# Kernel optimization log

Measured on AMD Instinct MI355X. Metric: run time of the kernel, lower is better.

## Reference

```python
import jax, jax.numpy as jnp
import numpy as np

MAX_SEGMENTS = 196
MAX_PIX = 400        # max_pixels_per_segment
C = 3                # n_channels
EMBED = 768


def setup_inputs() -> dict:
    key = jax.random.key(0)
    k1, k2, k3, k4 = jax.random.split(key, 4)
    B, H, W = 64, 224, 224
    img = jax.random.normal(k1, (B, C, H, W), jnp.float32)
    segments = jax.random.randint(k2, (B, H, W), 0, MAX_SEGMENTS).astype(jnp.int32)
    fan_in = C * MAX_PIX
    Wp = jax.random.normal(k3, (EMBED, fan_in), jnp.float32) / np.sqrt(fan_in)
    b = jax.random.normal(k4, (EMBED,), jnp.float32) * 0.01
    return {"img": img, "segments": segments, "W": Wp, "b": b}


def _gather_pad(img_flat, seg_flat):
    # img_flat: [C, P], seg_flat: [P] int32. Builds [S, C*MAX_PIX] padded buffer.
    P = seg_flat.shape[0]
    order = jnp.argsort(seg_flat, stable=True)          # stable -> keeps scan order (matches torch truncation)
    s = seg_flat[order]                                  # sorted segment ids, [P]
    counts = jnp.zeros((MAX_SEGMENTS,), jnp.int32).at[seg_flat].add(1)
    starts = jnp.concatenate([jnp.zeros((1,), jnp.int32),
                              jnp.cumsum(counts)[:-1].astype(jnp.int32)])
    rank = jnp.arange(P, dtype=jnp.int32) - starts[s]    # within-segment position
    valid = rank < MAX_PIX                               # truncate overly large segments
    rank_c = jnp.where(valid, rank, 0)
    vals = jnp.where(valid[:, None], img_flat.T[order], 0.0)  # [P, C]
    buf = jnp.zeros((MAX_SEGMENTS, C, MAX_PIX), img_flat.dtype)
    buf = buf.at[s, :, rank_c].add(vals)                 # invalid rows add zeros -> no-op
    # torch does pixels_in_segment.flatten() on (C, MAX_PIX) -> channel-major layout
    return buf.reshape(MAX_SEGMENTS, C * MAX_PIX)


def reference(img, segments, W, b):
    B = img.shape[0]
    img_flat = img.reshape(B, C, -1)          # [B, C, H*W]
    seg_flat = segments.reshape(B, -1)        # [B, H*W]
    feats = jax.vmap(_gather_pad)(img_flat, seg_flat)   # [B, S, C*MAX_PIX]
    return jnp.einsum('bsf,ef->bse', feats, W) + b      # nn.Linear
```

## Files before the change

kernel.cpp:

```cpp
#include <hip/hip_runtime.h>
#include <hip/hip_bf16.h>

#define B_      64
#define C_      3
#define H_      224
#define W_      224
#define P_      (H_*W_)
#define S_      196
#define MAXPIX  400
#define E_      768
#define K_      1200
#define KP_     1216
#define CHUNK_  512
#define NCH_    (P_/CHUNK_)
#define M_      (B_*S_)

typedef __attribute__((ext_vector_type(8))) short short8;
typedef __attribute__((ext_vector_type(4))) float f32x4;

__device__ inline unsigned short f2bf(float f) {
  union { float f; unsigned int u; } x; x.f = f;
  return (unsigned short)((x.u + 0x7fffu + ((x.u >> 16) & 1u)) >> 16);
}

__device__ inline int xcd_chunk(int wg, int nwg) {
  int q = nwg >> 3;
  return (wg & 7) * q + (wg >> 3);
}

__global__ void wconv_k(const float* __restrict__ Wf, unsigned short* __restrict__ Wb) {
  int idx = blockIdx.x * 256 + threadIdx.x;
  int e = idx / KP_, k = idx - e * KP_;
  float v = (k < K_) ? Wf[e * K_ + k] : 0.f;
  Wb[idx] = f2bf(v);
}

__global__ __launch_bounds__(512) void rank_k(const int* __restrict__ seg,
                                              int* __restrict__ hist,
                                              unsigned short* __restrict__ rloc) {
  int b = blockIdx.x / NCH_, ch = blockIdx.x % NCH_;
  int tid = threadIdx.x, wave = tid >> 6, lane = tid & 63;
  int p = ch * CHUNK_ + tid;
  int s = seg[b * P_ + p];

  __shared__ int lhist[8][S_];
  for (int i = tid; i < 8 * S_; i += 512) ((int*)lhist)[i] = 0;
  __syncthreads();

  int r = 0;
  #pragma unroll 1
  for (int j = 0; j < 64; ++j) {
    int sj = __shfl(s, j);
    r += (j < lane && sj == s) ? 1 : 0;
  }
  atomicAdd(&lhist[wave][s], 1);
  __syncthreads();

  int off = 0;
  for (int w2 = 0; w2 < wave; ++w2) off += lhist[w2][s];
  rloc[b * P_ + p] = (unsigned short)(off + r);

  if (tid < S_) {
    int t = 0;
    #pragma unroll
    for (int w2 = 0; w2 < 8; ++w2) t += lhist[w2][tid];
    hist[(b * NCH_ + ch) * S_ + tid] = t;
  }
}

__global__ __launch_bounds__(128) void prefix_k(int* __restrict__ hist, int* __restrict__ cnts) {
  int b = blockIdx.x / S_, s = blockIdx.x % S_;
  int t = threadIdx.x;
  __shared__ int sc[128];
  int v = (t < NCH_) ? hist[(b * NCH_ + t) * S_ + s] : 0;
  sc[t] = v;
  __syncthreads();
  #pragma unroll
  for (int off = 1; off < 128; off <<= 1) {
    int x = (t >= off) ? sc[t - off] : 0;
    __syncthreads();
    sc[t] += x;
    __syncthreads();
  }
  if (t < NCH_) hist[(b * NCH_ + t) * S_ + s] = sc[t] - v;
  if (t == NCH_ - 1) {
    int tot = sc[t];
    cnts[b * S_ + s] = tot < MAXPIX ? tot : MAXPIX;
  }
}

__global__ __launch_bounds__(256) void scatter_inv_k(const int* __restrict__ seg,
                                                     const int* __restrict__ starts,
                                                     const unsigned short* __restrict__ rloc,
                                                     unsigned short* __restrict__ inv) {
  int wg = xcd_chunk(blockIdx.x, B_ * (P_ / 256));
  int b = wg / (P_ / 256);
  int p = (wg % (P_ / 256)) * 256 + threadIdx.x;
  int s = seg[b * P_ + p];
  int rank = starts[(b * NCH_ + (p >> 9)) * S_ + s] + rloc[b * P_ + p];
  if (rank < MAXPIX)
    inv[(b * S_ + s) * MAXPIX + rank] = (unsigned short)p;
}

__global__ __launch_bounds__(256) void gather_k(const float* __restrict__ img,
                                                const unsigned short* __restrict__ inv,
                                                const int* __restrict__ cnts,
                                                unsigned short* __restrict__ feats) {
  int wg = xcd_chunk(blockIdx.x, M_);
  int b = wg / S_, s = wg % S_;
  int t = threadIdx.x;
  int cnt = cnts[b * S_ + s];
  const unsigned short* invrow = inv + (size_t)(b * S_ + s) * MAXPIX;
  unsigned short* frow = feats + (size_t)(b * S_ + s) * KP_;
  #pragma unroll
  for (int c = 0; c < C_; ++c) {
    const float* ic = img + ((size_t)b * C_ + c) * P_;
    for (int r = t; r < MAXPIX; r += 256) {
      int p = invrow[r];
      float v = (r < cnt) ? ic[p] : 0.f;
      frow[c * MAXPIX + r] = f2bf(v);
    }
  }
  if (t < KP_ - K_) frow[K_ + t] = 0;
}

__global__ __launch_bounds__(256) void gemm_k(const unsigned short* __restrict__ A,
                                              const unsigned short* __restrict__ Bw,
                                              const float* __restrict__ bias,
                                              float* __restrict__ out) {
  int bid;
  {
    int wg = blockIdx.x, q = 588 / 8, r = 588 % 8;
    int xcd = wg % 8, idx = wg / 8;
    bid = (xcd < r) ? xcd * (q + 1) + idx : r * (q + 1) + (xcd - r) * q + idx;
  }
  const int nb = bid % (E_ / 128);
  const int mb = bid / (E_ / 128);
  const int tid = threadIdx.x;
  const int w = tid >> 6, l = tid & 63;
  const int wr = w >> 1, wc = w & 1;

  __shared__ __align__(16) unsigned short As[128 * 32];
  __shared__ __align__(16) unsigned short Bs[128 * 32];

  f32x4 acc[4][4] = {};

  const int lrow = l >> 2;
  const int lcol = (l & 3) * 8;
  const int kk = (l >> 4) * 8;

  for (int k0 = 0; k0 < KP_; k0 += 32) {
    #pragma unroll
    for (int q = 0; q < 2; ++q) {
      int r = (w * 2 + q) * 16 + lrow;
      const unsigned short* ga = A + (size_t)(mb * 128 + r) * KP_ + k0 + lcol;
      __builtin_amdgcn_global_load_lds((const __attribute__((address_space(1))) unsigned int*)ga,
                                       (__attribute__((address_space(3))) unsigned int*)&As[(w * 2 + q) * 512],
                                       16, 0, 0);
      const unsigned short* gb = Bw + (size_t)(nb * 128 + r) * KP_ + k0 + lcol;
      __builtin_amdgcn_global_load_lds((const __attribute__((address_space(1))) unsigned int*)gb,
                                       (__attribute__((address_space(3))) unsigned int*)&Bs[(w * 2 + q) * 512],
                                       16, 0, 0);
    }
    __syncthreads();

    short8 af[4], bf[4];
    #pragma unroll
    for (int mi = 0; mi < 4; ++mi)
      af[mi] = *(const short8*)&As[(wr * 64 + mi * 16 + (l & 15)) * 32 + kk];
    #pragma unroll
    for (int ni = 0; ni < 4; ++ni)
      bf[ni] = *(const short8*)&Bs[(wc * 64 + ni * 16 + (l & 15)) * 32 + kk];
    #pragma unroll
    for (int mi = 0; mi < 4; ++mi)
      #pragma unroll
      for (int ni = 0; ni < 4; ++ni)
        acc[mi][ni] = __builtin_amdgcn_mfma_f32_16x16x32_bf16(af[mi], bf[ni], acc[mi][ni], 0, 0, 0);
    __syncthreads();
  }

  const int r0 = (l >> 4) * 4;
  const int c0 = l & 15;
  #pragma unroll
  for (int mi = 0; mi < 4; ++mi) {
    #pragma unroll
    for (int ni = 0; ni < 4; ++ni) {
      int col = nb * 128 + wc * 64 + ni * 16 + c0;
      float bv = bias[col];
      int row = mb * 128 + wr * 64 + mi * 16 + r0;
      #pragma unroll
      for (int r = 0; r < 4; ++r)
        out[(size_t)(row + r) * E_ + col] = acc[mi][ni][r] + bv;
    }
  }
}

extern "C" void kernel_launch(void* const* d_in, const int* in_sizes, int n_in,
                              void* d_out, int out_size, void* d_ws, size_t ws_size,
                              hipStream_t stream) {
  const float* img  = (const float*)d_in[0];
  const int*   seg  = (const int*)d_in[1];
  const float* Wf   = (const float*)d_in[2];
  const float* bias = (const float*)d_in[3];
  float* out = (float*)d_out;

  constexpr size_t WB_BYTES    = (size_t)E_ * KP_ * 2;
  constexpr size_t INV_BYTES   = (size_t)M_ * MAXPIX * 2;
  constexpr size_t CNT_BYTES   = (size_t)M_ * 4;
  constexpr size_t RLOC_BYTES  = (size_t)B_ * P_ * 2;
  char* ws = (char*)d_ws;
  unsigned short* Wb    = (unsigned short*)ws;
  unsigned short* inv   = (unsigned short*)(ws + WB_BYTES);
  int*            cnts  = (int*)(ws + WB_BYTES + INV_BYTES);
  unsigned short* feats = (unsigned short*)(ws + WB_BYTES + INV_BYTES + CNT_BYTES);
  unsigned short* rloc  = feats;
  int*            hist  = (int*)((char*)feats + RLOC_BYTES);

  wconv_k<<<(E_ * KP_) / 256, 256, 0, stream>>>(Wf, Wb);
  rank_k<<<B_ * NCH_, 512, 0, stream>>>(seg, hist, rloc);
  prefix_k<<<B_ * S_, 128, 0, stream>>>(hist, cnts);
  scatter_inv_k<<<B_ * (P_ / 256), 256, 0, stream>>>(seg, hist, rloc, inv);
  gather_k<<<M_, 256, 0, stream>>>(img, inv, cnts, feats);
  gemm_k<<<(M_ / 128) * (E_ / 128), 256, 0, stream>>>(feats, Wb, bias, out);
}
```

Baseline: 253.9 us.

## Scatter pixel values directly into pixel-major feature rows, dropping inverse-index gather

```diff
diff --git a/kernel.cpp b/kernel.cpp
--- a/kernel.cpp
+++ b/kernel.cpp
@@ -15,6 +15,7 @@
 #define NCH_    (P_/CHUNK_)
 #define M_      (B_*S_)
 
+
 typedef __attribute__((ext_vector_type(8))) short short8;
 typedef __attribute__((ext_vector_type(4))) float f32x4;
 
@@ -28,10 +29,21 @@
   return (wg & 7) * q + (wg >> 3);
 }
 
+__global__ void zero_k(int4* __restrict__ p, int n4) {
+  int i = blockIdx.x * blockDim.x + threadIdx.x;
+  int stride = gridDim.x * blockDim.x;
+  int4 z = make_int4(0, 0, 0, 0);
+  for (; i < n4; i += stride) p[i] = z;
+}
+
 __global__ void wconv_k(const float* __restrict__ Wf, unsigned short* __restrict__ Wb) {
   int idx = blockIdx.x * 256 + threadIdx.x;
   int e = idx / KP_, k = idx - e * KP_;
-  float v = (k < K_) ? Wf[e * K_ + k] : 0.f;
+  float v = 0.f;
+  if (k < K_) {
+    int r = k / 3, c = k - r * 3;
+    v = Wf[e * K_ + c * MAXPIX + r];
+  }
   Wb[idx] = f2bf(v);
 }
 
@@ -68,7 +80,7 @@
   }
 }
 
-__global__ __launch_bounds__(128) void prefix_k(int* __restrict__ hist, int* __restrict__ cnts) {
+__global__ __launch_bounds__(128) void prefix_k(int* __restrict__ hist) {
   int b = blockIdx.x / S_, s = blockIdx.x % S_;
   int t = threadIdx.x;
   __shared__ int sc[128];
@@ -83,45 +95,32 @@
     __syncthreads();
   }
   if (t < NCH_) hist[(b * NCH_ + t) * S_ + s] = sc[t] - v;
-  if (t == NCH_ - 1) {
-    int tot = sc[t];
-    cnts[b * S_ + s] = tot < MAXPIX ? tot : MAXPIX;
-  }
-}
-
-__global__ __launch_bounds__(256) void scatter_inv_k(const int* __restrict__ seg,
-                                                     const int* __restrict__ starts,
-                                                     const unsigned short* __restrict__ rloc,
-                                                     unsigned short* __restrict__ inv) {
+}
+
+__global__ __launch_bounds__(256) void scatter_vals_k(const float* __restrict__ img,
+                                                      const int* __restrict__ seg,
+                                                      const int* __restrict__ starts,
+                                                      const unsigned short* __restrict__ rloc,
+                                                      unsigned short* __restrict__ feats) {
   int wg = xcd_chunk(blockIdx.x, B_ * (P_ / 256));
   int b = wg / (P_ / 256);
   int p = (wg % (P_ / 256)) * 256 + threadIdx.x;
   int s = seg[b * P_ + p];
   int rank = starts[(b * NCH_ + (p >> 9)) * S_ + s] + rloc[b * P_ + p];
-  if (rank < MAXPIX)
-    inv[(b * S_ + s) * MAXPIX + rank] = (unsigned short)p;
-}
-
-__global__ __launch_bounds__(256) void gather_k(const float* __restrict__ img,
-                                                const unsigned short* __restrict__ inv,
-                                                const int* __restrict__ cnts,
-                                                unsigned short* __restrict__ feats) {
-  int wg = xcd_chunk(blockIdx.x, M_);
-  int b = wg / S_, s = wg % S_;
-  int t = threadIdx.x;
-  int cnt = cnts[b * S_ + s];
-  const unsigned short* invrow = inv + (size_t)(b * S_ + s) * MAXPIX;
-  unsigned short* frow = feats + (size_t)(b * S_ + s) * KP_;
-  #pragma unroll
-  for (int c = 0; c < C_; ++c) {
-    const float* ic = img + ((size_t)b * C_ + c) * P_;
-    for (int r = t; r < MAXPIX; r += 256) {
-      int p = invrow[r];
-      float v = (r < cnt) ? ic[p] : 0.f;
-      frow[c * MAXPIX + r] = f2bf(v);
+  if (rank < MAXPIX) {
+    const float* ib = img + (size_t)b * C_ * P_;
+    unsigned short c0 = f2bf(ib[p]);
+    unsigned short c1 = f2bf(ib[P_ + p]);
+    unsigned short c2 = f2bf(ib[2 * P_ + p]);
+    char* bp = (char*)(feats + (size_t)(b * S_ + s) * KP_) + 6 * (size_t)rank;
+    if (rank & 1) {
+      *(unsigned short*)bp = c0;
+      *(unsigned int*)(bp + 2) = (unsigned int)c1 | ((unsigned int)c2 << 16);
+    } else {
+      *(unsigned int*)bp = (unsigned int)c0 | ((unsigned int)c1 << 16);
+      *(unsigned short*)(bp + 4) = c2;
     }
   }
-  if (t < KP_ - K_) frow[K_ + t] = 0;
 }
 
 __global__ __launch_bounds__(256) void gemm_k(const unsigned short* __restrict__ A,
@@ -205,21 +204,18 @@
   float* out = (float*)d_out;
 
   constexpr size_t WB_BYTES    = (size_t)E_ * KP_ * 2;
-  constexpr size_t INV_BYTES   = (size_t)M_ * MAXPIX * 2;
-  constexpr size_t CNT_BYTES   = (size_t)M_ * 4;
+  constexpr size_t FEATS_BYTES = (size_t)M_ * KP_ * 2;
   constexpr size_t RLOC_BYTES  = (size_t)B_ * P_ * 2;
   char* ws = (char*)d_ws;
   unsigned short* Wb    = (unsigned short*)ws;
-  unsigned short* inv   = (unsigned short*)(ws + WB_BYTES);
-  int*            cnts  = (int*)(ws + WB_BYTES + INV_BYTES);
-  unsigned short* feats = (unsigned short*)(ws + WB_BYTES + INV_BYTES + CNT_BYTES);
-  unsigned short* rloc  = feats;
-  int*            hist  = (int*)((char*)feats + RLOC_BYTES);
-
+  unsigned short* feats = (unsigned short*)(ws + WB_BYTES);
+  unsigned short* rloc  = (unsigned short*)(ws + WB_BYTES + FEATS_BYTES);
+  int*            hist  = (int*)(ws + WB_BYTES + FEATS_BYTES + RLOC_BYTES);
+
+  zero_k<<<2048, 256, 0, stream>>>((int4*)feats, (int)(FEATS_BYTES / 16));
   wconv_k<<<(E_ * KP_) / 256, 256, 0, stream>>>(Wf, Wb);
   rank_k<<<B_ * NCH_, 512, 0, stream>>>(seg, hist, rloc);
-  prefix_k<<<B_ * S_, 128, 0, stream>>>(hist, cnts);
-  scatter_inv_k<<<B_ * (P_ / 256), 256, 0, stream>>>(seg, hist, rloc, inv);
-  gather_k<<<M_, 256, 0, stream>>>(img, inv, cnts, feats);
+  prefix_k<<<B_ * S_, 128, 0, stream>>>(hist);
+  scatter_vals_k<<<B_ * (P_ / 256), 256, 0, stream>>>(img, seg, hist, rloc, feats);
   gemm_k<<<(M_ / 128) * (E_ / 128), 256, 0, stream>>>(feats, Wb, bias, out);
 }
```

Measured after the change: 238.3 us. 1.07x faster.
